# Kernel tuning notes

Measured on AMD Instinct MI355X. Metric: run time of the kernel, lower is better.

Reference implementation:

```python
import jax, jax.numpy as jnp
import numpy as np

MAX_USERS = 100000
T = 2            # edge_type_count
D = 100          # edge_dim
B = 512
IN_DIM = 200
OUT_DIM = 200
PARTS = [[3, 15], [3, 15, 105, 945]]   # per-schema neighbor partition sizes
RAND_PARTS = [3, 15]
TOTAL_P = sum(PARTS[0]) + sum(PARTS[1])


def _layernorm(x, g, b, eps=1e-6):
    mu = x.mean(axis=-1, keepdims=True)
    var = ((x - mu) ** 2).mean(axis=-1, keepdims=True)
    return (x - mu) / jnp.sqrt(var + eps) * g + b


def _mha(x, Wq, Wk, Wv, Wf, g, b):
    # single-head attention over the second-to-last axis (n_head=1, d_k=d_v=D).
    # NOTE: original only layer-norms q (k, v use the raw input); residual add at end.
    residual = x
    q = _layernorm(x, g, b) @ Wq
    k = x @ Wk
    v = x @ Wv
    attn = jax.nn.softmax(jnp.einsum('...qd,...kd->...qk', q / jnp.sqrt(D), k), axis=-1)
    out = jnp.einsum('...qk,...kd->...qd', attn, v) @ Wf
    return out + residual, attn


def _mean_agg(Ws, Wn, self_x, neigh_x):
    # GraphSAGE-style mean aggregator: relu(concat(self @ Ws, mean(neigh) @ Wn)).
    # neigh_x has shape [N*r, D]; reshape to [N, r, D] and mean over the fanout r.
    n, d = self_x.shape
    neigh_mean = neigh_x.reshape(n, -1, d).mean(axis=1)
    return jax.nn.relu(jnp.concatenate([self_x @ Ws, neigh_mean @ Wn], axis=-1))


def _schema_view(idx, parts, Wself, Wneigh, type_embed, nodeids, neigh_s):
    # neigh_s: [B, T, sum(parts)] node ids for meta-path idx. Returns [B, T, D].
    # Faithful to type_embed[neigh][:, :, :, :, idx, :][:, t, :, t, :] but gathers
    # only the needed (type t, schema idx) slice instead of the huge dense tensor.
    chunks = jnp.split(neigh_s, np.cumsum(parts)[:-1].tolist(), axis=2)
    specs = []
    for t in range(T):
        feats = [type_embed[nodeids, t, idx]]                    # [B, D]
        for c in chunks:
            feats.append(type_embed[c[:, t, :], t, idx].reshape(-1, D))
        for l in range(len(parts)):
            feats = [_mean_agg(Wself[l], Wneigh[l], feats[k], feats[k + 1])
                     for k in range(len(feats) - 1)]
        specs.append(feats[0])
    return jnp.stack(specs, axis=1)


def setup_inputs() -> dict:
    ks = jax.random.split(jax.random.key(0), 32)
    unif = lambda i, s: jax.random.uniform(ks[i], s, dtype=jnp.float32, minval=-1.0, maxval=1.0)
    nrm = lambda i, s, sc=0.1: jax.random.normal(ks[i], s, dtype=jnp.float32) * sc
    inp = {}
    inp['nodeids'] = jax.random.randint(ks[0], (B,), 0, MAX_USERS)
    inp['edgetype'] = jnp.stack([jnp.arange(B), jax.random.randint(ks[1], (B,), 0, T)])
    inp['neighbors'] = jax.random.randint(ks[2], (B, T, TOTAL_P), 0, MAX_USERS)
    inp['random_neighbors'] = jax.random.randint(ks[3], (B, sum(RAND_PARTS)), 0, MAX_USERS)
    inp['base_embed'] = unif(4, (MAX_USERS, IN_DIM))
    inp['type_embed'] = unif(5, (MAX_USERS, T, len(PARTS), D))
    inp['rw_embed'] = unif(6, (MAX_USERS, D))
    inp['reflect'] = nrm(7, (T, D, OUT_DIM), 1.0 / float(np.sqrt(IN_DIM)))
    inp['agg0_self'] = nrm(8, (2, D, D // 2)); inp['agg0_neigh'] = nrm(9, (2, D, D // 2))
    inp['agg1_self'] = nrm(10, (4, D, D // 2)); inp['agg1_neigh'] = nrm(11, (4, D, D // 2))
    inp['rand_self'] = nrm(12, (2, D, D // 2)); inp['rand_neigh'] = nrm(13, (2, D, D // 2))
    inp['vWq'] = nrm(14, (D, D)); inp['vWk'] = nrm(15, (D, D)); inp['vWv'] = nrm(16, (D, D)); inp['vWf'] = nrm(17, (D, D))
    inp['vg'] = jnp.ones((D,), jnp.float32); inp['vb'] = jnp.zeros((D,), jnp.float32)
    inp['mWq'] = nrm(18, (D, D)); inp['mWk'] = nrm(19, (D, D)); inp['mWv'] = nrm(20, (D, D)); inp['mWf'] = nrm(21, (D, D))
    inp['mg'] = jnp.ones((D,), jnp.float32); inp['mb'] = jnp.zeros((D,), jnp.float32)
    return inp


def reference(nodeids, edgetype, neighbors, random_neighbors, base_embed, type_embed,
              rw_embed, reflect, agg0_self, agg0_neigh, agg1_self, agg1_neigh,
              rand_self, rand_neigh, vWq, vWk, vWv, vWf, vg, vb,
              mWq, mWk, mWv, mWf, mg, mb):
    # per-metapath views [B, T, D]
    spec0 = _schema_view(0, PARTS[0], agg0_self, agg0_neigh, type_embed, nodeids,
                         neighbors[:, :, :sum(PARTS[0])])
    spec1 = _schema_view(1, PARTS[1], agg1_self, agg1_neigh, type_embed, nodeids,
                         neighbors[:, :, sum(PARTS[0]):])
    # random-walk view [B, D]
    feats = [rw_embed[nodeids]]
    for c in jnp.split(random_neighbors, np.cumsum(RAND_PARTS)[:-1].tolist(), axis=1):
        feats.append(rw_embed[c].reshape(-1, D))
    for l in range(len(RAND_PARTS)):
        feats = [_mean_agg(rand_self[l], rand_neigh[l], feats[k], feats[k + 1])
                 for k in range(len(feats) - 1)]
    rview = feats[0]
    mv = jnp.stack([spec0, spec1], axis=1)                                   # [B, 2, T, D]
    mv = jnp.concatenate([mv, jnp.broadcast_to(rview[:, None, None, :], (B, 1, T, D))], axis=1)  # [B, 3, T, D]
    mv, _ = _mha(mv, vWq, vWk, vWv, vWf, vg, vb)                             # view attn over type axis T
    mt, _ = _mha(jnp.swapaxes(mv, 1, 2), mWq, mWk, mWv, mWf, mg, mb)         # meta attn over view axis
    pooled = jnp.swapaxes(mt, 1, 2).mean(axis=1)                             # [B, T, D]
    sel = pooled[edgetype[0], edgetype[1]]                                   # [B, D]
    out = jnp.einsum('bd,bdo->bo', sel, reflect[edgetype[1]])                # [B, OUT_DIM]
    res = base_embed[nodeids] + out
    return res / jnp.maximum(jnp.linalg.norm(res, axis=1, keepdims=True), 1e-12)
```

## Files before the change

kernel.cpp:

```cpp
#include <hip/hip_runtime.h>
#include <math.h>


#define NBATCH 512
#define TOTALP 1086
#define RPB 32
#define XSTR 204

struct Seg {
  const float* emb;
  const float* selfp;
  const float* neighp;
  const int*   ids_s;
  const int*   ids_n;
  const float* Ws;
  const float* Wn;
  float*       outp;
  int ss, so;
  int ns, no;
  int estride;
  int ostride;
  int c;
  int r;
  int blk_begin;
};

struct KArgs { Seg seg[14]; int n; };

__global__ __launch_bounds__(256) void agg_kernel(KArgs P) {
  __shared__ float xsh[RPB * XSTR];
  __shared__ int   ids_s_sh[RPB];
  __shared__ int   ids_n_sh[RPB * 9];

  const int blk = blockIdx.x, tid = threadIdx.x;
  int si = 0;
  for (int i = 1; i < P.n; ++i)
    if (blk >= P.seg[i].blk_begin) si = i;
  const Seg sg = P.seg[si];
  const int j0 = (blk - sg.blk_begin) * RPB;
  const int c = sg.c, r = sg.r;

  if (sg.emb) {
    if (tid < RPB) {
      int j = j0 + tid, b = j / c, pos = j - b * c;
      ids_s_sh[tid] = sg.ids_s[(long)b * sg.ss + sg.so + pos];
    }
    for (int u = tid; u < RPB * r; u += 256) {
      int row = u / r, q = u - row * r;
      int j = j0 + row, b = j / c, pos = j - b * c;
      ids_n_sh[u] = sg.ids_n[(long)b * sg.ns + sg.no + pos * r + q];
    }
    __syncthreads();
  }

  const float rinv = 1.f / (float)r;
  for (int u = tid; u < RPB * 25; u += 256) {
    int row = u / 25, q4 = (u - row * 25) * 4;
    float sx, sy, sz, sw, mx = 0.f, my = 0.f, mz = 0.f, mw = 0.f;
    if (sg.emb) {
      const float4 s4 = *(const float4*)(sg.emb + (long)ids_s_sh[row] * sg.estride + q4);
      sx = s4.x; sy = s4.y; sz = s4.z; sw = s4.w;
      for (int rr = 0; rr < r; ++rr) {
        const float4 t = *(const float4*)(sg.emb + (long)ids_n_sh[row * r + rr] * sg.estride + q4);
        mx += t.x; my += t.y; mz += t.z; mw += t.w;
      }
    } else {
      long j = j0 + row;
      const float4 s4 = *(const float4*)(sg.selfp + j * 100 + q4);
      sx = s4.x; sy = s4.y; sz = s4.z; sw = s4.w;
      for (int rr = 0; rr < r; ++rr) {
        const float4 t = *(const float4*)(sg.neighp + (j * r + rr) * 100 + q4);
        mx += t.x; my += t.y; mz += t.z; mw += t.w;
      }
    }
    float4 sv; sv.x = sx; sv.y = sy; sv.z = sz; sv.w = sw;
    float4 mv; mv.x = mx * rinv; mv.y = my * rinv; mv.z = mz * rinv; mv.w = mw * rinv;
    *(float4*)&xsh[row * XSTR + q4]       = sv;
    *(float4*)&xsh[row * XSTR + 100 + q4] = mv;
  }
  __syncthreads();

  if (tid < 208) {
    const int rg = tid / 26, hq = tid - rg * 26;
    const int half = hq / 13, q = hq - half * 13;
    const int col = 4 * q;
    const float* W = half ? sg.Wn : sg.Ws;
    const float* xb = &xsh[(rg * 4) * XSTR + half * 100];
    float acc[4][4];
#pragma unroll
    for (int i = 0; i < 4; ++i) { acc[i][0] = acc[i][1] = acc[i][2] = acc[i][3] = 0.f; }
    if (q < 12) {
#pragma unroll 2
      for (int e = 0; e < 100; ++e) {
        const float4 wv = *(const float4*)&W[e * 50 + col];
#pragma unroll
        for (int i = 0; i < 4; ++i) {
          const float a = xb[i * XSTR + e];
          acc[i][0] = fmaf(a, wv.x, acc[i][0]);
          acc[i][1] = fmaf(a, wv.y, acc[i][1]);
          acc[i][2] = fmaf(a, wv.z, acc[i][2]);
          acc[i][3] = fmaf(a, wv.w, acc[i][3]);
        }
      }
    } else {
#pragma unroll 2
      for (int e = 0; e < 100; ++e) {
        const float2 wv = *(const float2*)&W[e * 50 + 48];
#pragma unroll
        for (int i = 0; i < 4; ++i) {
          const float a = xb[i * XSTR + e];
          acc[i][0] = fmaf(a, wv.x, acc[i][0]);
          acc[i][1] = fmaf(a, wv.y, acc[i][1]);
        }
      }
    }
    const int ocol = half * 50 + col;
    for (int i = 0; i < 4; ++i) {
      const long j = j0 + rg * 4 + i;
      float* op = sg.outp + j * (long)sg.ostride + ocol;
      if (q < 12) {
        float4 o;
        o.x = fmaxf(acc[i][0], 0.f); o.y = fmaxf(acc[i][1], 0.f);
        o.z = fmaxf(acc[i][2], 0.f); o.w = fmaxf(acc[i][3], 0.f);
        *(float4*)op = o;
      } else {
        float2 o;
        o.x = fmaxf(acc[i][0], 0.f); o.y = fmaxf(acc[i][1], 0.f);
        *(float2*)op = o;
      }
    }
  }
}

__device__ __forceinline__ float wave_sum_bcast(float p) {
#pragma unroll
  for (int off = 32; off; off >>= 1) p += __shfl_down(p, off);
  return __shfl(p, 0);
}

__global__ __launch_bounds__(256) void attn_final_kernel(
    const float* __restrict__ spec, const float* __restrict__ rview,
    const int* __restrict__ nodeids, const int* __restrict__ edgetype,
    const float* __restrict__ base_embed, const float* __restrict__ reflect,
    const float* __restrict__ vWq, const float* __restrict__ vWk,
    const float* __restrict__ vWv, const float* __restrict__ vWf,
    const float* __restrict__ vg, const float* __restrict__ vb,
    const float* __restrict__ mWq, const float* __restrict__ mWk,
    const float* __restrict__ mWv, const float* __restrict__ mWf,
    const float* __restrict__ mg, const float* __restrict__ mb,
    float* __restrict__ out)
{
  __shared__ float xs[600], lnb[300], qq[300], kk[300], vv[300], ot[300];
  __shared__ float sc[9], musd[6], pooled[100], r200[200], nrmv[1];
  const int b = blockIdx.x, tid = threadIdx.x;
  const int et = edgetype[NBATCH + b];
  const int nid = nodeids[b];

  for (int o = tid; o < 600; o += 256) {
    int v = o / 200, rem = o - v * 200;
    xs[o] = (v < 2) ? spec[(long)b * 400 + o] : rview[(long)b * 100 + (rem % 100)];
  }
  __syncthreads();

  for (int v = 0; v < 3; ++v) {
    float* xq = xs + v * 200 + et * 100;
    if (tid < 64) {
      float p = (tid < 50) ? xq[tid] + xq[tid + 50] : 0.f;
      p = wave_sum_bcast(p);
      float mu = p * 0.01f, vr = 0.f;
      if (tid < 50) { float a = xq[tid] - mu, c2 = xq[tid + 50] - mu; vr = a * a + c2 * c2; }
      vr = wave_sum_bcast(vr);
      if (tid == 0) { musd[0] = mu; musd[1] = rsqrtf(vr * 0.01f + 1e-6f); }
    }
    __syncthreads();
    if (tid < 100) lnb[tid] = (xq[tid] - musd[0]) * musd[1] * vg[tid] + vb[tid];
    __syncthreads();
    for (int o = tid; o < 500; o += 256) {
      const int m = o / 100, d = o - m * 100;
      const float* xr; const float* W; float* dst;
      if (m == 0)      { xr = lnb;                          W = vWq; dst = qq; }
      else if (m <= 2) { xr = xs + v * 200 + (m - 1) * 100; W = vWk; dst = kk + (m - 1) * 100; }
      else             { xr = xs + v * 200 + (m - 3) * 100; W = vWv; dst = vv + (m - 3) * 100; }
      float a = 0.f;
      for (int e = 0; e < 100; ++e) a = fmaf(xr[e], W[e * 100 + d], a);
      dst[d] = a;
    }
    __syncthreads();
    if (tid < 2) {
      float s = 0.f;
      for (int d = 0; d < 100; ++d) s = fmaf(qq[d], kk[tid * 100 + d], s);
      sc[tid] = s * 0.1f;
    }
    __syncthreads();
    if (tid == 0) {
      float mx = fmaxf(sc[0], sc[1]);
      float e0 = __expf(sc[0] - mx), e1 = __expf(sc[1] - mx);
      float inv = 1.f / (e0 + e1);
      sc[0] = e0 * inv; sc[1] = e1 * inv;
    }
    __syncthreads();
    if (tid < 100) ot[tid] = sc[0] * vv[tid] + sc[1] * vv[100 + tid];
    __syncthreads();
    if (tid < 100) {
      float a = 0.f;
      for (int e = 0; e < 100; ++e) a = fmaf(ot[e], vWf[e * 100 + tid], a);
      xq[tid] += a;
    }
    __syncthreads();
  }

  {
    const int w = tid >> 6, l = tid & 63;
    if (w < 3) {
      const float* xr = xs + w * 200 + et * 100;
      float p = (l < 50) ? xr[l] + xr[l + 50] : 0.f;
      p = wave_sum_bcast(p);
      float mu = p * 0.01f, vr = 0.f;
      if (l < 50) { float a = xr[l] - mu, c2 = xr[l + 50] - mu; vr = a * a + c2 * c2; }
      vr = wave_sum_bcast(vr);
      if (l == 0) { musd[w * 2] = mu; musd[w * 2 + 1] = rsqrtf(vr * 0.01f + 1e-6f); }
    }
    __syncthreads();
    for (int o = tid; o < 300; o += 256) {
      int i = o / 100, d = o - i * 100;
      lnb[o] = (xs[i * 200 + et * 100 + d] - musd[i * 2]) * musd[i * 2 + 1] * mg[d] + mb[d];
    }
    __syncthreads();
    for (int o = tid; o < 900; o += 256) {
      const int m = o / 300, rr = (o - m * 300) / 100, d = o - m * 300 - rr * 100;
      const float* xr = (m == 0) ? (lnb + rr * 100) : (xs + rr * 200 + et * 100);
      const float* W  = (m == 0) ? mWq : (m == 1 ? mWk : mWv);
      float a = 0.f;
      for (int e = 0; e < 100; ++e) a = fmaf(xr[e], W[e * 100 + d], a);
      float* dst = (m == 0) ? qq : (m == 1 ? kk : vv);
      dst[rr * 100 + d] = a;
    }
    __syncthreads();
    if (tid < 9) {
      int i = tid / 3, u = tid - i * 3;
      float s = 0.f;
      for (int d = 0; d < 100; ++d) s = fmaf(qq[i * 100 + d], kk[u * 100 + d], s);
      sc[tid] = s * 0.1f;
    }
    __syncthreads();
    if (tid < 3) {
      float mx = fmaxf(sc[tid * 3], fmaxf(sc[tid * 3 + 1], sc[tid * 3 + 2]));
      float e0 = __expf(sc[tid * 3] - mx), e1 = __expf(sc[tid * 3 + 1] - mx),
            e2 = __expf(sc[tid * 3 + 2] - mx);
      float inv = 1.f / (e0 + e1 + e2);
      sc[tid * 3] = e0 * inv; sc[tid * 3 + 1] = e1 * inv; sc[tid * 3 + 2] = e2 * inv;
    }
    __syncthreads();
    for (int o = tid; o < 300; o += 256) {
      int i = o / 100, d = o - i * 100;
      ot[o] = sc[i * 3] * vv[d] + sc[i * 3 + 1] * vv[100 + d] + sc[i * 3 + 2] * vv[200 + d];
    }
    __syncthreads();
    for (int o = tid; o < 300; o += 256) {
      int i = o / 100, d = o - i * 100;
      float a = 0.f;
      for (int e = 0; e < 100; ++e) a = fmaf(ot[i * 100 + e], mWf[e * 100 + d], a);
      xs[i * 200 + et * 100 + d] += a;
    }
    __syncthreads();
  }

  if (tid < 100)
    pooled[tid] = (xs[et * 100 + tid] + xs[200 + et * 100 + tid] +
                   xs[400 + et * 100 + tid]) * (1.f / 3.f);
  __syncthreads();
  if (tid < 200) {
    float a = base_embed[(long)nid * 200 + tid];
    const float* rf = reflect + (long)et * 20000 + tid;
    for (int d = 0; d < 100; ++d) a = fmaf(pooled[d], rf[d * 200], a);
    r200[tid] = a;
  }
  __syncthreads();
  if (tid < 64) {
    float p = r200[tid] * r200[tid] + r200[tid + 64] * r200[tid + 64]
            + r200[tid + 128] * r200[tid + 128];
    if (tid < 8) p += r200[tid + 192] * r200[tid + 192];
    p = wave_sum_bcast(p);
    if (tid == 0) nrmv[0] = 1.f / fmaxf(sqrtf(p), 1e-12f);
  }
  __syncthreads();
  if (tid < 200) out[(long)b * 200 + tid] = r200[tid] * nrmv[0];
}

extern "C" void kernel_launch(void* const* d_in, const int* in_sizes, int n_in,
                              void* d_out, int out_size, void* d_ws, size_t ws_size,
                              hipStream_t stream) {
  (void)in_sizes; (void)n_in; (void)out_size; (void)ws_size;
  const int*   nodeids          = (const int*)d_in[0];
  const int*   edgetype         = (const int*)d_in[1];
  const int*   neighbors        = (const int*)d_in[2];
  const int*   random_neighbors = (const int*)d_in[3];
  const float* base_embed       = (const float*)d_in[4];
  const float* type_embed       = (const float*)d_in[5];
  const float* rw_embed         = (const float*)d_in[6];
  const float* reflect          = (const float*)d_in[7];
  const float* agg0_self        = (const float*)d_in[8];
  const float* agg0_neigh       = (const float*)d_in[9];
  const float* agg1_self        = (const float*)d_in[10];
  const float* agg1_neigh       = (const float*)d_in[11];
  const float* rand_self        = (const float*)d_in[12];
  const float* rand_neigh       = (const float*)d_in[13];
  const float* vWq = (const float*)d_in[14];
  const float* vWk = (const float*)d_in[15];
  const float* vWv = (const float*)d_in[16];
  const float* vWf = (const float*)d_in[17];
  const float* vg  = (const float*)d_in[18];
  const float* vb  = (const float*)d_in[19];
  const float* mWq = (const float*)d_in[20];
  const float* mWk = (const float*)d_in[21];
  const float* mWv = (const float*)d_in[22];
  const float* mWf = (const float*)d_in[23];
  const float* mg  = (const float*)d_in[24];
  const float* mb  = (const float*)d_in[25];

  float* ws = (float*)d_ws;
  const long S1r = 147L * NBATCH;
  auto rp = [&](long rows) { return ws + rows * 100; };
  float* spec_f  = ws + 306L * NBATCH * 100;
  float* rview_f = spec_f + (long)NBATCH * 400;

  const int  OFF1[4] = {18, 21, 36, 141};
  const int  FAN1[4] = {3, 5, 7, 9};
  const int  C1[4]   = {1, 3, 15, 105};
  const long CUM1[4]  = {0, 1, 4, 19};
  const long CUM1b[3] = {0, 1, 4};

  KArgs A; long acc = 0;
  auto addg = [&](const float* emb, int estride,
                  const int* isrc, int ss, int so, int c,
                  const int* insrc, int nstr, int no, int r,
                  const float* Ws, const float* Wn, float* outp, int ostride) {
    Seg& s = A.seg[A.n++];
    s.emb = emb; s.selfp = nullptr; s.neighp = nullptr;
    s.ids_s = isrc; s.ids_n = insrc;
    s.Ws = Ws; s.Wn = Wn; s.outp = outp;
    s.ss = ss; s.so = so; s.ns = nstr; s.no = no;
    s.estride = estride; s.ostride = ostride;
    s.c = c; s.r = r; s.blk_begin = (int)acc;
    acc += (long)c * NBATCH / RPB;
  };
  auto addd = [&](const float* selfp, const float* neighp, int c, int r,
                  const float* Ws, const float* Wn, float* outp, int ostride) {
    Seg& s = A.seg[A.n++];
    s.emb = nullptr; s.selfp = selfp; s.neighp = neighp;
    s.ids_s = nullptr; s.ids_n = nullptr;
    s.Ws = Ws; s.Wn = Wn; s.outp = outp;
    s.ss = 0; s.so = 0; s.ns = 0; s.no = 0; s.estride = 0; s.ostride = ostride;
    s.c = c; s.r = r; s.blk_begin = (int)acc;
    acc += (long)c * NBATCH / RPB;
  };

  A.n = 0; acc = 0;
  for (int t = 0; t < 2; ++t)
    for (int k = 0; k < 4; ++k) {
      const float* emb = type_embed + (t * 2 + 1) * 100;
      if (k == 0)
        addg(emb, 400, nodeids, 1, 0, 1,
             neighbors, 2 * TOTALP, t * TOTALP + OFF1[k], FAN1[k],
             agg1_self, agg1_neigh, rp(t * S1r + CUM1[k] * NBATCH), 100);
      else
        addg(emb, 400, neighbors, 2 * TOTALP, t * TOTALP + OFF1[k - 1], C1[k],
             neighbors, 2 * TOTALP, t * TOTALP + OFF1[k], FAN1[k],
             agg1_self, agg1_neigh, rp(t * S1r + CUM1[k] * NBATCH), 100);
    }
  for (int t = 0; t < 2; ++t)
    for (int k = 0; k < 2; ++k) {
      const float* emb = type_embed + (t * 2 + 0) * 100;
      long obase = 294L * NBATCH + (long)t * 4 * NBATCH + (k == 0 ? 0 : 1) * NBATCH;
      if (k == 0)
        addg(emb, 400, nodeids, 1, 0, 1,
             neighbors, 2 * TOTALP, t * TOTALP + 0, 3,
             agg0_self, agg0_neigh, rp(obase), 100);
      else
        addg(emb, 400, neighbors, 2 * TOTALP, t * TOTALP + 0, 3,
             neighbors, 2 * TOTALP, t * TOTALP + 3, 5,
             agg0_self, agg0_neigh, rp(obase), 100);
    }
  for (int k = 0; k < 2; ++k) {
    long obase = 302L * NBATCH + (k == 0 ? 0 : 1) * NBATCH;
    if (k == 0)
      addg(rw_embed, 100, nodeids, 1, 0, 1,
           random_neighbors, 18, 0, 3, rand_self, rand_neigh, rp(obase), 100);
    else
      addg(rw_embed, 100, random_neighbors, 18, 0, 3,
           random_neighbors, 18, 3, 5, rand_self, rand_neigh, rp(obase), 100);
  }
  agg_kernel<<<dim3((unsigned)acc), dim3(256), 0, stream>>>(A);

  A.n = 0; acc = 0;
  for (int t = 0; t < 2; ++t)
    for (int k = 0; k < 3; ++k)
      addd(rp(t * S1r + CUM1[k] * NBATCH), rp(t * S1r + CUM1[k + 1] * NBATCH),
           C1[k], FAN1[k], agg1_self + 5000, agg1_neigh + 5000,
           rp(t * S1r + 124L * NBATCH + CUM1b[k] * NBATCH), 100);
  for (int t = 0; t < 2; ++t)
    addd(rp(294L * NBATCH + (long)t * 4 * NBATCH),
         rp(294L * NBATCH + (long)t * 4 * NBATCH + NBATCH),
         1, 3, agg0_self + 5000, agg0_neigh + 5000, spec_f + t * 100, 400);
  addd(rp(302L * NBATCH), rp(303L * NBATCH), 1, 3,
       rand_self + 5000, rand_neigh + 5000, rview_f, 100);
  agg_kernel<<<dim3((unsigned)acc), dim3(256), 0, stream>>>(A);

  A.n = 0; acc = 0;
  for (int t = 0; t < 2; ++t)
    for (int k = 0; k < 2; ++k)
      addd(rp(t * S1r + 124L * NBATCH + CUM1b[k] * NBATCH),
           rp(t * S1r + 124L * NBATCH + CUM1b[k + 1] * NBATCH),
           C1[k], FAN1[k], agg1_self + 10000, agg1_neigh + 10000,
           rp(t * S1r + 143L * NBATCH + (k == 0 ? 0 : 1) * NBATCH), 100);
  agg_kernel<<<dim3((unsigned)acc), dim3(256), 0, stream>>>(A);

  A.n = 0; acc = 0;
  for (int t = 0; t < 2; ++t)
    addd(rp(t * S1r + 143L * NBATCH), rp(t * S1r + 144L * NBATCH),
         1, 3, agg1_self + 15000, agg1_neigh + 15000,
         spec_f + 200 + t * 100, 400);
  agg_kernel<<<dim3((unsigned)acc), dim3(256), 0, stream>>>(A);

  attn_final_kernel<<<dim3(NBATCH), dim3(256), 0, stream>>>(
      spec_f, rview_f, nodeids, edgetype, base_embed, reflect,
      vWq, vWk, vWv, vWf, vg, vb, mWq, mWk, mWv, mWf, mg, mb,
      (float*)d_out);
}
```

Before: 707.6 us.

## Fuse upper aggregation levels into per-batch tail kernel with attention

Replaces the three dense agg_kernel launches for the upper GraphSAGE levels with a per-sample tail kernel. It loads each sample's first-level outputs into shared memory, runs the remaining mean-aggregate and matmul levels there, then does the attention and final projection. This removes three launches and the global round trips of the intermediate levels. The cost is that each of the 512 blocks re-reads the weight matrices and uses a large shared-memory footprint (~68 KB), which limits occupancy. It also unrolls the inner matmul loops by 4 with float4 activation reads in both kernels.

```diff
diff --git a/kernel.cpp b/kernel.cpp
--- a/kernel.cpp
+++ b/kernel.cpp
@@ -9,8 +9,6 @@
 
 struct Seg {
   const float* emb;
-  const float* selfp;
-  const float* neighp;
   const int*   ids_s;
   const int*   ids_n;
   const float* Ws;
@@ -19,7 +17,6 @@
   int ss, so;
   int ns, no;
   int estride;
-  int ostride;
   int c;
   int r;
   int blk_begin;
@@ -40,42 +37,28 @@
   const int j0 = (blk - sg.blk_begin) * RPB;
   const int c = sg.c, r = sg.r;
 
-  if (sg.emb) {
-    if (tid < RPB) {
-      int j = j0 + tid, b = j / c, pos = j - b * c;
-      ids_s_sh[tid] = sg.ids_s[(long)b * sg.ss + sg.so + pos];
-    }
-    for (int u = tid; u < RPB * r; u += 256) {
-      int row = u / r, q = u - row * r;
-      int j = j0 + row, b = j / c, pos = j - b * c;
-      ids_n_sh[u] = sg.ids_n[(long)b * sg.ns + sg.no + pos * r + q];
-    }
-    __syncthreads();
-  }
+  if (tid < RPB) {
+    int j = j0 + tid, b = j / c, pos = j - b * c;
+    ids_s_sh[tid] = sg.ids_s[(long)b * sg.ss + sg.so + pos];
+  }
+  for (int u = tid; u < RPB * r; u += 256) {
+    int row = u / r, q = u - row * r;
+    int j = j0 + row, b = j / c, pos = j - b * c;
+    ids_n_sh[u] = sg.ids_n[(long)b * sg.ns + sg.no + pos * r + q];
+  }
+  __syncthreads();
 
   const float rinv = 1.f / (float)r;
   for (int u = tid; u < RPB * 25; u += 256) {
     int row = u / 25, q4 = (u - row * 25) * 4;
-    float sx, sy, sz, sw, mx = 0.f, my = 0.f, mz = 0.f, mw = 0.f;
-    if (sg.emb) {
-      const float4 s4 = *(const float4*)(sg.emb + (long)ids_s_sh[row] * sg.estride + q4);
-      sx = s4.x; sy = s4.y; sz = s4.z; sw = s4.w;
-      for (int rr = 0; rr < r; ++rr) {
-        const float4 t = *(const float4*)(sg.emb + (long)ids_n_sh[row * r + rr] * sg.estride + q4);
-        mx += t.x; my += t.y; mz += t.z; mw += t.w;
-      }
-    } else {
-      long j = j0 + row;
-      const float4 s4 = *(const float4*)(sg.selfp + j * 100 + q4);
-      sx = s4.x; sy = s4.y; sz = s4.z; sw = s4.w;
-      for (int rr = 0; rr < r; ++rr) {
-        const float4 t = *(const float4*)(sg.neighp + (j * r + rr) * 100 + q4);
-        mx += t.x; my += t.y; mz += t.z; mw += t.w;
-      }
-    }
-    float4 sv; sv.x = sx; sv.y = sy; sv.z = sz; sv.w = sw;
+    const float4 s4 = *(const float4*)(sg.emb + (long)ids_s_sh[row] * sg.estride + q4);
+    float mx = 0.f, my = 0.f, mz = 0.f, mw = 0.f;
+    for (int rr = 0; rr < r; ++rr) {
+      const float4 t = *(const float4*)(sg.emb + (long)ids_n_sh[row * r + rr] * sg.estride + q4);
+      mx += t.x; my += t.y; mz += t.z; mw += t.w;
+    }
     float4 mv; mv.x = mx * rinv; mv.y = my * rinv; mv.z = mz * rinv; mv.w = mw * rinv;
-    *(float4*)&xsh[row * XSTR + q4]       = sv;
+    *(float4*)&xsh[row * XSTR + q4]       = s4;
     *(float4*)&xsh[row * XSTR + 100 + q4] = mv;
   }
   __syncthreads();
@@ -91,33 +74,57 @@
     for (int i = 0; i < 4; ++i) { acc[i][0] = acc[i][1] = acc[i][2] = acc[i][3] = 0.f; }
     if (q < 12) {
 #pragma unroll 2
-      for (int e = 0; e < 100; ++e) {
-        const float4 wv = *(const float4*)&W[e * 50 + col];
+      for (int eb = 0; eb < 100; eb += 4) {
+        const float4 w0 = *(const float4*)&W[(eb + 0) * 50 + col];
+        const float4 w1 = *(const float4*)&W[(eb + 1) * 50 + col];
+        const float4 w2 = *(const float4*)&W[(eb + 2) * 50 + col];
+        const float4 w3 = *(const float4*)&W[(eb + 3) * 50 + col];
 #pragma unroll
         for (int i = 0; i < 4; ++i) {
-          const float a = xb[i * XSTR + e];
-          acc[i][0] = fmaf(a, wv.x, acc[i][0]);
-          acc[i][1] = fmaf(a, wv.y, acc[i][1]);
-          acc[i][2] = fmaf(a, wv.z, acc[i][2]);
-          acc[i][3] = fmaf(a, wv.w, acc[i][3]);
+          const float4 xv = *(const float4*)&xb[i * XSTR + eb];
+          acc[i][0] = fmaf(xv.x, w0.x, acc[i][0]);
+          acc[i][0] = fmaf(xv.y, w1.x, acc[i][0]);
+          acc[i][0] = fmaf(xv.z, w2.x, acc[i][0]);
+          acc[i][0] = fmaf(xv.w, w3.x, acc[i][0]);
+          acc[i][1] = fmaf(xv.x, w0.y, acc[i][1]);
+          acc[i][1] = fmaf(xv.y, w1.y, acc[i][1]);
+          acc[i][1] = fmaf(xv.z, w2.y, acc[i][1]);
+          acc[i][1] = fmaf(xv.w, w3.y, acc[i][1]);
+          acc[i][2] = fmaf(xv.x, w0.z, acc[i][2]);
+          acc[i][2] = fmaf(xv.y, w1.z, acc[i][2]);
+          acc[i][2] = fmaf(xv.z, w2.z, acc[i][2]);
+          acc[i][2] = fmaf(xv.w, w3.z, acc[i][2]);
+          acc[i][3] = fmaf(xv.x, w0.w, acc[i][3]);
+          acc[i][3] = fmaf(xv.y, w1.w, acc[i][3]);
+          acc[i][3] = fmaf(xv.z, w2.w, acc[i][3]);
+          acc[i][3] = fmaf(xv.w, w3.w, acc[i][3]);
         }
       }
     } else {
 #pragma unroll 2
-      for (int e = 0; e < 100; ++e) {
-        const float2 wv = *(const float2*)&W[e * 50 + 48];
+      for (int eb = 0; eb < 100; eb += 4) {
+        const float2 w0 = *(const float2*)&W[(eb + 0) * 50 + 48];
+        const float2 w1 = *(const float2*)&W[(eb + 1) * 50 + 48];
+        const float2 w2 = *(const float2*)&W[(eb + 2) * 50 + 48];
+        const float2 w3 = *(const float2*)&W[(eb + 3) * 50 + 48];
 #pragma unroll
         for (int i = 0; i < 4; ++i) {
-          const float a = xb[i * XSTR + e];
-          acc[i][0] = fmaf(a, wv.x, acc[i][0]);
-          acc[i][1] = fmaf(a, wv.y, acc[i][1]);
+          const float4 xv = *(const float4*)&xb[i * XSTR + eb];
+          acc[i][0] = fmaf(xv.x, w0.x, acc[i][0]);
+          acc[i][0] = fmaf(xv.y, w1.x, acc[i][0]);
+          acc[i][0] = fmaf(xv.z, w2.x, acc[i][0]);
+          acc[i][0] = fmaf(xv.w, w3.x, acc[i][0]);
+          acc[i][1] = fmaf(xv.x, w0.y, acc[i][1]);
+          acc[i][1] = fmaf(xv.y, w1.y, acc[i][1]);
+          acc[i][1] = fmaf(xv.z, w2.y, acc[i][1]);
+          acc[i][1] = fmaf(xv.w, w3.y, acc[i][1]);
         }
       }
     }
     const int ocol = half * 50 + col;
     for (int i = 0; i < 4; ++i) {
       const long j = j0 + rg * 4 + i;
-      float* op = sg.outp + j * (long)sg.ostride + ocol;
+      float* op = sg.outp + j * 100L + ocol;
       if (q < 12) {
         float4 o;
         o.x = fmaxf(acc[i][0], 0.f); o.y = fmaxf(acc[i][1], 0.f);
@@ -138,10 +145,61 @@
   return __shfl(p, 0);
 }
 
-__global__ __launch_bounds__(256) void attn_final_kernel(
-    const float* __restrict__ spec, const float* __restrict__ rview,
+struct LvlMap { int jb1, jb2, sb0, sb1, sb2, nb0, nb1, nb2, r0, r1, r2; };
+
+__device__ __forceinline__ void do_level(
+    const float* src, float* dst, float* msh, int nrows, LvlMap m,
+    const float* Ws, const float* Wn, int tid)
+{
+  for (int u = tid; u < nrows * 25; u += 256) {
+    const int j = u / 25, d4 = (u - j * 25) * 4;
+    const int g  = (j >= m.jb1) + (j >= m.jb2);
+    const int jb = (g == 0) ? 0 : (g == 1 ? m.jb1 : m.jb2);
+    const int nb = (g == 0) ? m.nb0 : (g == 1 ? m.nb1 : m.nb2);
+    const int r  = (g == 0) ? m.r0 : (g == 1 ? m.r1 : m.r2);
+    const int nbase = nb + (j - jb) * r;
+    float ax = 0.f, ay = 0.f, az = 0.f, aw = 0.f;
+    for (int rr = 0; rr < r; ++rr) {
+      const float4 t = *(const float4*)&src[(nbase + rr) * 100 + d4];
+      ax += t.x; ay += t.y; az += t.z; aw += t.w;
+    }
+    const float rinv = 1.f / (float)r;
+    float4 o; o.x = ax * rinv; o.y = ay * rinv; o.z = az * rinv; o.w = aw * rinv;
+    *(float4*)&msh[j * 100 + d4] = o;
+  }
+  __syncthreads();
+  for (int u = tid; u < nrows * 100; u += 256) {
+    const int j = u / 100, o = u - j * 100;
+    const int g  = (j >= m.jb1) + (j >= m.jb2);
+    const int jb = (g == 0) ? 0 : (g == 1 ? m.jb1 : m.jb2);
+    const int sb = (g == 0) ? m.sb0 : (g == 1 ? m.sb1 : m.sb2);
+    const int srow = sb + (j - jb);
+    const float* x = (o < 50) ? &src[srow * 100] : &msh[j * 100];
+    const float* W = (o < 50) ? Ws : Wn;
+    const int col = (o < 50) ? o : o - 50;
+    float a = 0.f;
+#pragma unroll 2
+    for (int eb = 0; eb < 100; eb += 4) {
+      const float w0 = W[(eb + 0) * 50 + col];
+      const float w1 = W[(eb + 1) * 50 + col];
+      const float w2 = W[(eb + 2) * 50 + col];
+      const float w3 = W[(eb + 3) * 50 + col];
+      const float4 xv = *(const float4*)&x[eb];
+      a = fmaf(xv.x, w0, a); a = fmaf(xv.y, w1, a);
+      a = fmaf(xv.z, w2, a); a = fmaf(xv.w, w3, a);
+    }
+    dst[j * 100 + o] = fmaxf(a, 0.f);
+  }
+  __syncthreads();
+}
+
+__global__ __launch_bounds__(256) void tail_kernel(
+    const float* __restrict__ ws,
     const int* __restrict__ nodeids, const int* __restrict__ edgetype,
     const float* __restrict__ base_embed, const float* __restrict__ reflect,
+    const float* __restrict__ agg0_self, const float* __restrict__ agg0_neigh,
+    const float* __restrict__ agg1_self, const float* __restrict__ agg1_neigh,
+    const float* __restrict__ rand_self, const float* __restrict__ rand_neigh,
     const float* __restrict__ vWq, const float* __restrict__ vWk,
     const float* __restrict__ vWv, const float* __restrict__ vWf,
     const float* __restrict__ vg, const float* __restrict__ vb,
@@ -150,17 +208,76 @@
     const float* __restrict__ mg, const float* __restrict__ mb,
     float* __restrict__ out)
 {
+  __shared__ float ash[12400];
+  __shared__ float hsh[1900];
+  __shared__ float psh[400];
+  __shared__ float msh[1900];
   __shared__ float xs[600], lnb[300], qq[300], kk[300], vv[300], ot[300];
   __shared__ float sc[9], musd[6], pooled[100], r200[200], nrmv[1];
+
   const int b = blockIdx.x, tid = threadIdx.x;
   const int et = edgetype[NBATCH + b];
   const int nid = nodeids[b];
 
-  for (int o = tid; o < 600; o += 256) {
-    int v = o / 200, rem = o - v * 200;
-    xs[o] = (v < 2) ? spec[(long)b * 400 + o] : rview[(long)b * 100 + (rem % 100)];
-  }
-  __syncthreads();
+  const int C1k[4]  = {1, 3, 15, 105};
+  const int CUM1[4] = {0, 1, 4, 19};
+
+  for (int t = 0; t < 2; ++t) {
+    const long tbase = (long)t * 147 * NBATCH;
+    for (int k = 0; k < 4; ++k) {
+      const float* gsrc = ws + (tbase + (long)CUM1[k] * NBATCH + (long)b * C1k[k]) * 100;
+      float* ldst = ash + CUM1[k] * 100;
+      for (int u = tid; u < C1k[k] * 25; u += 256)
+        *(float4*)&ldst[u * 4] = *(const float4*)&gsrc[u * 4];
+    }
+    __syncthreads();
+    LvlMap m1; m1.jb1 = 1; m1.jb2 = 4;
+    m1.sb0 = 0; m1.sb1 = 1; m1.sb2 = 4;
+    m1.nb0 = 1; m1.nb1 = 4; m1.nb2 = 19;
+    m1.r0 = 3; m1.r1 = 5; m1.r2 = 7;
+    do_level(ash, hsh, msh, 19, m1, agg1_self + 5000, agg1_neigh + 5000, tid);
+    LvlMap m2; m2.jb1 = 1; m2.jb2 = 999;
+    m2.sb0 = 0; m2.sb1 = 1; m2.sb2 = 0;
+    m2.nb0 = 1; m2.nb1 = 4; m2.nb2 = 0;
+    m2.r0 = 3; m2.r1 = 5; m2.r2 = 1;
+    do_level(hsh, psh, msh, 4, m2, agg1_self + 10000, agg1_neigh + 10000, tid);
+    LvlMap m3; m3.jb1 = 999; m3.jb2 = 999;
+    m3.sb0 = 0; m3.sb1 = 0; m3.sb2 = 0;
+    m3.nb0 = 1; m3.nb1 = 0; m3.nb2 = 0;
+    m3.r0 = 3; m3.r1 = 1; m3.r2 = 1;
+    do_level(psh, xs + 200 + t * 100, msh, 1, m3,
+             agg1_self + 15000, agg1_neigh + 15000, tid);
+  }
+
+  for (int t = 0; t < 2; ++t) {
+    const long base = 294L * NBATCH + (long)t * 4 * NBATCH;
+    for (int u = tid; u < 25; u += 256)
+      *(float4*)&ash[u * 4] = *(const float4*)&ws[(base + b) * 100 + u * 4];
+    for (int u = tid; u < 75; u += 256)
+      *(float4*)&ash[100 + u * 4] =
+          *(const float4*)&ws[(base + NBATCH + (long)b * 3) * 100 + u * 4];
+    __syncthreads();
+    LvlMap m; m.jb1 = 999; m.jb2 = 999;
+    m.sb0 = 0; m.sb1 = 0; m.sb2 = 0; m.nb0 = 1; m.nb1 = 0; m.nb2 = 0;
+    m.r0 = 3; m.r1 = 1; m.r2 = 1;
+    do_level(ash, xs + t * 100, msh, 1, m, agg0_self + 5000, agg0_neigh + 5000, tid);
+  }
+
+  {
+    const long base = 302L * NBATCH;
+    for (int u = tid; u < 25; u += 256)
+      *(float4*)&ash[u * 4] = *(const float4*)&ws[(base + b) * 100 + u * 4];
+    for (int u = tid; u < 75; u += 256)
+      *(float4*)&ash[100 + u * 4] =
+          *(const float4*)&ws[(base + NBATCH + (long)b * 3) * 100 + u * 4];
+    __syncthreads();
+    LvlMap m; m.jb1 = 999; m.jb2 = 999;
+    m.sb0 = 0; m.sb1 = 0; m.sb2 = 0; m.nb0 = 1; m.nb1 = 0; m.nb2 = 0;
+    m.r0 = 3; m.r1 = 1; m.r2 = 1;
+    do_level(ash, xs + 400, msh, 1, m, rand_self + 5000, rand_neigh + 5000, tid);
+    if (tid < 100) xs[500 + tid] = xs[400 + tid];
+    __syncthreads();
+  }
 
   for (int v = 0; v < 3; ++v) {
     float* xq = xs + v * 200 + et * 100;
@@ -176,13 +293,19 @@
     if (tid < 100) lnb[tid] = (xq[tid] - musd[0]) * musd[1] * vg[tid] + vb[tid];
     __syncthreads();
     for (int o = tid; o < 500; o += 256) {
-      const int m = o / 100, d = o - m * 100;
+      const int mm = o / 100, d = o - mm * 100;
       const float* xr; const float* W; float* dst;
-      if (m == 0)      { xr = lnb;                          W = vWq; dst = qq; }
-      else if (m <= 2) { xr = xs + v * 200 + (m - 1) * 100; W = vWk; dst = kk + (m - 1) * 100; }
-      else             { xr = xs + v * 200 + (m - 3) * 100; W = vWv; dst = vv + (m - 3) * 100; }
+      if (mm == 0)      { xr = lnb;                           W = vWq; dst = qq; }
+      else if (mm <= 2) { xr = xs + v * 200 + (mm - 1) * 100; W = vWk; dst = kk + (mm - 1) * 100; }
+      else              { xr = xs + v * 200 + (mm - 3) * 100; W = vWv; dst = vv + (mm - 3) * 100; }
       float a = 0.f;
-      for (int e = 0; e < 100; ++e) a = fmaf(xr[e], W[e * 100 + d], a);
+#pragma unroll 2
+      for (int eb = 0; eb < 100; eb += 4) {
+        const float w0 = W[(eb + 0) * 100 + d], w1 = W[(eb + 1) * 100 + d];
+        const float w2 = W[(eb + 2) * 100 + d], w3 = W[(eb + 3) * 100 + d];
+        a = fmaf(xr[eb], w0, a); a = fmaf(xr[eb + 1], w1, a);
+        a = fmaf(xr[eb + 2], w2, a); a = fmaf(xr[eb + 3], w3, a);
+      }
       dst[d] = a;
     }
     __syncthreads();
@@ -227,12 +350,18 @@
     }
     __syncthreads();
     for (int o = tid; o < 900; o += 256) {
-      const int m = o / 300, rr = (o - m * 300) / 100, d = o - m * 300 - rr * 100;
-      const float* xr = (m == 0) ? (lnb + rr * 100) : (xs + rr * 200 + et * 100);
-      const float* W  = (m == 0) ? mWq : (m == 1 ? mWk : mWv);
+      const int mm = o / 300, rr = (o - mm * 300) / 100, d = o - mm * 300 - rr * 100;
+      const float* xr = (mm == 0) ? (lnb + rr * 100) : (xs + rr * 200 + et * 100);
+      const float* W  = (mm == 0) ? mWq : (mm == 1 ? mWk : mWv);
       float a = 0.f;
-      for (int e = 0; e < 100; ++e) a = fmaf(xr[e], W[e * 100 + d], a);
-      float* dst = (m == 0) ? qq : (m == 1 ? kk : vv);
+#pragma unroll 2
+      for (int eb = 0; eb < 100; eb += 4) {
+        const float w0 = W[(eb + 0) * 100 + d], w1 = W[(eb + 1) * 100 + d];
+        const float w2 = W[(eb + 2) * 100 + d], w3 = W[(eb + 3) * 100 + d];
+        a = fmaf(xr[eb], w0, a); a = fmaf(xr[eb + 1], w1, a);
+        a = fmaf(xr[eb + 2], w2, a); a = fmaf(xr[eb + 3], w3, a);
+      }
+      float* dst = (mm == 0) ? qq : (mm == 1 ? kk : vv);
       dst[rr * 100 + d] = a;
     }
     __syncthreads();
@@ -260,7 +389,12 @@
       int i = o / 100, d = o - i * 100;
       float a = 0.f;
       for (int e = 0; e < 100; ++e) a = fmaf(ot[i * 100 + e], mWf[e * 100 + d], a);
-      xs[i * 200 + et * 100 + d] += a;
+      lnb[o] = a;
+    }
+    __syncthreads();
+    for (int o = tid; o < 300; o += 256) {
+      int i = o / 100, d = o - i * 100;
+      xs[i * 200 + et * 100 + d] += lnb[o];
     }
     __syncthreads();
   }
@@ -272,6 +406,7 @@
   if (tid < 200) {
     float a = base_embed[(long)nid * 200 + tid];
     const float* rf = reflect + (long)et * 20000 + tid;
+#pragma unroll 2
     for (int d = 0; d < 100; ++d) a = fmaf(pooled[d], rf[d * 200], a);
     r200[tid] = a;
   }
@@ -321,37 +456,22 @@
   float* ws = (float*)d_ws;
   const long S1r = 147L * NBATCH;
   auto rp = [&](long rows) { return ws + rows * 100; };
-  float* spec_f  = ws + 306L * NBATCH * 100;
-  float* rview_f = spec_f + (long)NBATCH * 400;
 
   const int  OFF1[4] = {18, 21, 36, 141};
   const int  FAN1[4] = {3, 5, 7, 9};
   const int  C1[4]   = {1, 3, 15, 105};
-  const long CUM1[4]  = {0, 1, 4, 19};
-  const long CUM1b[3] = {0, 1, 4};
+  const long CUM1[4] = {0, 1, 4, 19};
 
   KArgs A; long acc = 0;
   auto addg = [&](const float* emb, int estride,
                   const int* isrc, int ss, int so, int c,
                   const int* insrc, int nstr, int no, int r,
-                  const float* Ws, const float* Wn, float* outp, int ostride) {
+                  const float* Ws, const float* Wn, float* outp) {
     Seg& s = A.seg[A.n++];
-    s.emb = emb; s.selfp = nullptr; s.neighp = nullptr;
-    s.ids_s = isrc; s.ids_n = insrc;
+    s.emb = emb; s.ids_s = isrc; s.ids_n = insrc;
     s.Ws = Ws; s.Wn = Wn; s.outp = outp;
     s.ss = ss; s.so = so; s.ns = nstr; s.no = no;
-    s.estride = estride; s.ostride = ostride;
-    s.c = c; s.r = r; s.blk_begin = (int)acc;
-    acc += (long)c * NBATCH / RPB;
-  };
-  auto addd = [&](const float* selfp, const float* neighp, int c, int r,
-                  const float* Ws, const float* Wn, float* outp, int ostride) {
-    Seg& s = A.seg[A.n++];
-    s.emb = nullptr; s.selfp = selfp; s.neighp = neighp;
-    s.ids_s = nullptr; s.ids_n = nullptr;
-    s.Ws = Ws; s.Wn = Wn; s.outp = outp;
-    s.ss = 0; s.so = 0; s.ns = 0; s.no = 0; s.estride = 0; s.ostride = ostride;
-    s.c = c; s.r = r; s.blk_begin = (int)acc;
+    s.estride = estride; s.c = c; s.r = r; s.blk_begin = (int)acc;
     acc += (long)c * NBATCH / RPB;
   };
 
@@ -362,11 +482,11 @@
       if (k == 0)
         addg(emb, 400, nodeids, 1, 0, 1,
              neighbors, 2 * TOTALP, t * TOTALP + OFF1[k], FAN1[k],
-             agg1_self, agg1_neigh, rp(t * S1r + CUM1[k] * NBATCH), 100);
+             agg1_self, agg1_neigh, rp(t * S1r + CUM1[k] * NBATCH));
       else
         addg(emb, 400, neighbors, 2 * TOTALP, t * TOTALP + OFF1[k - 1], C1[k],
              neighbors, 2 * TOTALP, t * TOTALP + OFF1[k], FAN1[k],
-             agg1_self, agg1_neigh, rp(t * S1r + CUM1[k] * NBATCH), 100);
+             agg1_self, agg1_neigh, rp(t * S1r + CUM1[k] * NBATCH));
     }
   for (int t = 0; t < 2; ++t)
     for (int k = 0; k < 2; ++k) {
@@ -375,55 +495,26 @@
       if (k == 0)
         addg(emb, 400, nodeids, 1, 0, 1,
              neighbors, 2 * TOTALP, t * TOTALP + 0, 3,
-             agg0_self, agg0_neigh, rp(obase), 100);
+             agg0_self, agg0_neigh, rp(obase));
       else
         addg(emb, 400, neighbors, 2 * TOTALP, t * TOTALP + 0, 3,
              neighbors, 2 * TOTALP, t * TOTALP + 3, 5,
-             agg0_self, agg0_neigh, rp(obase), 100);
+             agg0_self, agg0_neigh, rp(obase));
     }
   for (int k = 0; k < 2; ++k) {
     long obase = 302L * NBATCH + (k == 0 ? 0 : 1) * NBATCH;
     if (k == 0)
       addg(rw_embed, 100, nodeids, 1, 0, 1,
-           random_neighbors, 18, 0, 3, rand_self, rand_neigh, rp(obase), 100);
+           random_neighbors, 18, 0, 3, rand_self, rand_neigh, rp(obase));
     else
       addg(rw_embed, 100, random_neighbors, 18, 0, 3,
-           random_neighbors, 18, 3, 5, rand_self, rand_neigh, rp(obase), 100);
+           random_neighbors, 18, 3, 5, rand_self, rand_neigh, rp(obase));
   }
   agg_kernel<<<dim3((unsigned)acc), dim3(256), 0, stream>>>(A);
 
-  A.n = 0; acc = 0;
-  for (int t = 0; t < 2; ++t)
-    for (int k = 0; k < 3; ++k)
-      addd(rp(t * S1r + CUM1[k] * NBATCH), rp(t * S1r + CUM1[k + 1] * NBATCH),
-           C1[k], FAN1[k], agg1_self + 5000, agg1_neigh + 5000,
-           rp(t * S1r + 124L * NBATCH + CUM1b[k] * NBATCH), 100);
-  for (int t = 0; t < 2; ++t)
-    addd(rp(294L * NBATCH + (long)t * 4 * NBATCH),
-         rp(294L * NBATCH + (long)t * 4 * NBATCH + NBATCH),
-         1, 3, agg0_self + 5000, agg0_neigh + 5000, spec_f + t * 100, 400);
-  addd(rp(302L * NBATCH), rp(303L * NBATCH), 1, 3,
-       rand_self + 5000, rand_neigh + 5000, rview_f, 100);
-  agg_kernel<<<dim3((unsigned)acc), dim3(256), 0, stream>>>(A);
-
-  A.n = 0; acc = 0;
-  for (int t = 0; t < 2; ++t)
-    for (int k = 0; k < 2; ++k)
-      addd(rp(t * S1r + 124L * NBATCH + CUM1b[k] * NBATCH),
-           rp(t * S1r + 124L * NBATCH + CUM1b[k + 1] * NBATCH),
-           C1[k], FAN1[k], agg1_self + 10000, agg1_neigh + 10000,
-           rp(t * S1r + 143L * NBATCH + (k == 0 ? 0 : 1) * NBATCH), 100);
-  agg_kernel<<<dim3((unsigned)acc), dim3(256), 0, stream>>>(A);
-
-  A.n = 0; acc = 0;
-  for (int t = 0; t < 2; ++t)
-    addd(rp(t * S1r + 143L * NBATCH), rp(t * S1r + 144L * NBATCH),
-         1, 3, agg1_self + 15000, agg1_neigh + 15000,
-         spec_f + 200 + t * 100, 400);
-  agg_kernel<<<dim3((unsigned)acc), dim3(256), 0, stream>>>(A);
-
-  attn_final_kernel<<<dim3(NBATCH), dim3(256), 0, stream>>>(
-      spec_f, rview_f, nodeids, edgetype, base_embed, reflect,
+  tail_kernel<<<dim3(NBATCH), dim3(256), 0, stream>>>(
+      ws, nodeids, edgetype, base_embed, reflect,
+      agg0_self, agg0_neigh, agg1_self, agg1_neigh, rand_self, rand_neigh,
       vWq, vWk, vWv, vWf, vg, vb, mWq, mWk, mWv, mWf, mg, mb,
       (float*)d_out);
 }
```

Measured after the change: 709.3 us. No clear change (+0.2%).
